# Optimization experiments

Hardware: AMD Instinct MI355X
Metric: run time of the kernel (lower is better)

The kernel has to match this reference:

```python
import jax, jax.numpy as jnp
import numpy as np

DIM = 768
NUM_HEADS = 12
HEAD_DIM = DIM // NUM_HEADS
H = W = 64
RANK = 4
LORA_SCALING = 1.0 / RANK  # lora_alpha(=1) / r


def setup_inputs() -> dict:
    key = jax.random.key(0)
    ks = jax.random.split(key, 11)
    s = 0.02
    return {
        "x": jax.random.normal(ks[0], (1, H, W, DIM), dtype=jnp.float32),
        "W_qkv": jax.random.normal(ks[1], (3 * DIM, DIM), dtype=jnp.float32) * s,
        "b_qkv": jax.random.normal(ks[2], (3 * DIM,), dtype=jnp.float32) * s,
        "A_q": jax.random.normal(ks[3], (RANK, DIM), dtype=jnp.float32) * s,
        "B_q": jax.random.normal(ks[4], (DIM, RANK), dtype=jnp.float32) * s,
        "A_v": jax.random.normal(ks[5], (RANK, DIM), dtype=jnp.float32) * s,
        "B_v": jax.random.normal(ks[6], (DIM, RANK), dtype=jnp.float32) * s,
        "rel_h": jax.random.normal(ks[7], (2 * H - 1, HEAD_DIM), dtype=jnp.float32) * s,
        "rel_w": jax.random.normal(ks[8], (2 * W - 1, HEAD_DIM), dtype=jnp.float32) * s,
        "W_proj": jax.random.normal(ks[9], (DIM, DIM), dtype=jnp.float32) * s,
        "b_proj": jax.random.normal(ks[10], (DIM,), dtype=jnp.float32) * s,
    }


def _get_rel_pos(size, rel_pos):
    # q_size == k_size == size; relative coords indexed into (2*size-1, head_dim)
    coords = jnp.arange(size)[:, None] - jnp.arange(size)[None, :] + (size - 1)
    return rel_pos[coords]  # (size, size, head_dim)


def reference(x, W_qkv, b_qkv, A_q, B_q, A_v, B_v, rel_h, rel_w, W_proj, b_proj):
    B, h, w, dim = x.shape
    nh, hd = NUM_HEADS, HEAD_DIM
    scale = hd ** -0.5
    n = h * w
    xf = x.reshape(B, n, dim)

    # LoRA-merged QKV: base linear + low-rank deltas on q and v thirds only
    qkv = xf @ W_qkv.T + b_qkv  # (B, n, 3*dim)
    dq = ((xf @ A_q.T) @ B_q.T) * LORA_SCALING
    dv = ((xf @ A_v.T) @ B_v.T) * LORA_SCALING
    qkv = qkv.at[..., :dim].add(dq).at[..., 2 * dim:].add(dv)

    qkv = qkv.reshape(B, n, 3, nh, hd).transpose(2, 0, 3, 1, 4).reshape(3, B * nh, n, hd)
    q, k, v = qkv[0], qkv[1], qkv[2]  # each (B*nh, n, hd)

    attn = (q * scale) @ jnp.swapaxes(k, -2, -1)  # (B*nh, n, n)

    # decomposed relative position bias (SAM style)
    Rh = _get_rel_pos(h, rel_h)  # (h, h, hd)
    Rw = _get_rel_pos(w, rel_w)  # (w, w, hd)
    r_q = q.reshape(B * nh, h, w, hd)
    bias_h = jnp.einsum("bhwc,hkc->bhwk", r_q, Rh)  # (B*nh, h, w, h)
    bias_w = jnp.einsum("bhwc,wkc->bhwk", r_q, Rw)  # (B*nh, h, w, w)
    attn = (attn.reshape(B * nh, h, w, h, w)
            + bias_h[:, :, :, :, None]
            + bias_w[:, :, :, None, :]).reshape(B * nh, n, n)

    attn = jax.nn.softmax(attn, axis=-1)
    out = (attn @ v).reshape(B, nh, h, w, hd).transpose(0, 2, 3, 1, 4).reshape(B, h, w, dim)
    return out @ W_proj.T + b_proj
```

## Files before the change

### kernel.cpp

```cpp
#include <hip/hip_runtime.h>

#define NTOK 4096
#define DIMD 768
#define NHD  12
#define HDD  64
#define DK   800

typedef float  f32x2  __attribute__((ext_vector_type(2)));
typedef float  f32x4  __attribute__((ext_vector_type(4)));
typedef float  f32x16 __attribute__((ext_vector_type(16)));
typedef short  s16x8  __attribute__((ext_vector_type(8)));

#define MFMA16(a, b, c) __builtin_amdgcn_mfma_f32_16x16x32_bf16(a, b, c, 0, 0, 0)
#define MFMA32(a, b, c) __builtin_amdgcn_mfma_f32_32x32x16_bf16(a, b, c, 0, 0, 0)

#if __has_builtin(__builtin_amdgcn_exp2f)
#define EXP2(x) __builtin_amdgcn_exp2f(x)
#else
#define EXP2(x) exp2f(x)
#endif

__device__ inline short f2b(float f) {
  unsigned u = __float_as_uint(f);
  u += 0x7FFFu + ((u >> 16) & 1u);
  return (short)(u >> 16);
}
__device__ inline float b2f(short s) {
  return __uint_as_float(((unsigned)(unsigned short)s) << 16);
}
__device__ inline void gl_lds16(const short* g, short* l) {
  __builtin_amdgcn_global_load_lds(
      (const __attribute__((address_space(1))) unsigned int*)g,
      (__attribute__((address_space(3))) unsigned int*)l, 16, 0, 0);
}


__global__ __launch_bounds__(64)
void k_prep_w(const float* __restrict__ Wqkv, const float* __restrict__ Bq,
              const float* __restrict__ Bv, const float* __restrict__ Wp,
              short* __restrict__ we, short* __restrict__ wpb) {
  const int j = blockIdx.x;
  const int l = threadIdx.x;
  if (j < 2304) {
#pragma unroll
    for (int k = 0; k < 12; ++k)
      we[(size_t)j * DK + l + 64 * k] = f2b(Wqkv[(size_t)j * DIMD + l + 64 * k]);
    if (l < 32) {
      int c = 768 + l;
      short v = 0;
      if (l < 4) {
        if (j < 768) v = f2b(Bq[j * 4 + l]);
      } else if (l < 8) {
        if (j >= 1536) v = f2b(Bv[(j - 1536) * 4 + (l - 4)]);
      }
      we[(size_t)j * DK + c] = v;
    }
  } else {
    const int jr = j - 2304;
#pragma unroll
    for (int k = 0; k < 12; ++k)
      wpb[(size_t)jr * DIMD + l + 64 * k] =
          f2b(Wp[(size_t)jr * DIMD + l + 64 * k]);
  }
}

__global__ __launch_bounds__(64)
void k_prep_x(const float* __restrict__ x, const float* __restrict__ Aq,
              const float* __restrict__ Av, short* __restrict__ xe) {
  const int i = blockIdx.x;
  const int l = threadIdx.x;
  float xv[12];
#pragma unroll
  for (int k = 0; k < 12; ++k) xv[k] = x[(size_t)i * DIMD + l + 64 * k];
#pragma unroll
  for (int k = 0; k < 12; ++k)
    xe[(size_t)i * DK + l + 64 * k] = f2b(xv[k]);
  float a8[8];
#pragma unroll
  for (int o = 0; o < 8; ++o) {
    const float* A = (o < 4) ? (Aq + o * DIMD) : (Av + (o - 4) * DIMD);
    float acc = 0.f;
#pragma unroll
    for (int k = 0; k < 12; ++k) acc = fmaf(xv[k], A[l + 64 * k], acc);
#pragma unroll
    for (int off = 32; off; off >>= 1) acc += __shfl_xor(acc, off, 64);
    a8[o] = acc;
  }
  if (l < 32) {
    float v = 0.f;
#pragma unroll
    for (int o = 0; o < 8; ++o)
      if (l == o) v = 0.25f * a8[o];
    xe[(size_t)i * DK + 768 + l] = (l < 8) ? f2b(v) : (short)0;
  }
}

__global__ __launch_bounds__(256)
void k_qkv(const short* __restrict__ xe, const short* __restrict__ we,
           const float* __restrict__ bqkv, short* __restrict__ qkvb,
           short* __restrict__ vtb) {
  const int j0 = blockIdx.x * 128;
  const int i0 = blockIdx.y * 128;
  __shared__ short As[128 * 32];
  __shared__ short Bs[128 * 32];
  __shared__ short Cs[128 * 130];
  const int t = threadIdx.x, lane = t & 63, w = t >> 6;
  const int l15 = lane & 15, quad = lane >> 4;
  const int wm = w >> 1, wn = w & 1;

  f32x4 acc[4][4];
#pragma unroll
  for (int a = 0; a < 4; ++a)
#pragma unroll
    for (int b = 0; b < 4; ++b) acc[a][b] = (f32x4){0.f, 0.f, 0.f, 0.f};

  for (int kk = 0; kk < DK; kk += 32) {
    __syncthreads();
#pragma unroll
    for (int rep = 0; rep < 2; ++rep) {
      int c = rep * 256 + w * 64 + lane;
      gl_lds16(xe + (size_t)(i0 + (c >> 2)) * DK + kk + (c & 3) * 8,
               &As[(rep * 256 + w * 64) * 8]);
      gl_lds16(we + (size_t)(j0 + (c >> 2)) * DK + kk + (c & 3) * 8,
               &Bs[(rep * 256 + w * 64) * 8]);
    }
    __syncthreads();
    s16x8 af[4], bf[4];
#pragma unroll
    for (int mt = 0; mt < 4; ++mt)
      af[mt] = *(const s16x8*)&As[(wm * 64 + mt * 16 + l15) * 32 + quad * 8];
#pragma unroll
    for (int nt = 0; nt < 4; ++nt)
      bf[nt] = *(const s16x8*)&Bs[(wn * 64 + nt * 16 + l15) * 32 + quad * 8];
#pragma unroll
    for (int mt = 0; mt < 4; ++mt)
#pragma unroll
      for (int nt = 0; nt < 4; ++nt)
        acc[mt][nt] = MFMA16(af[mt], bf[nt], acc[mt][nt]);
  }

  const int which = j0 / DIMD;
  float bj[4];
#pragma unroll
  for (int nt = 0; nt < 4; ++nt) bj[nt] = bqkv[j0 + wn * 64 + nt * 16 + l15];

#pragma unroll
  for (int mt = 0; mt < 4; ++mt)
#pragma unroll
    for (int r = 0; r < 4; ++r) {
      const int row = wm * 64 + mt * 16 + quad * 4 + r;
#pragma unroll
      for (int nt = 0; nt < 4; ++nt) {
        const int col = wn * 64 + nt * 16 + l15;
        Cs[row * 130 + col] = f2b(acc[mt][nt][r] + bj[nt]);
      }
    }
  __syncthreads();
  const int base_head = (j0 - which * DIMD) >> 6;
  if (which != 2) {
#pragma unroll
    for (int rp = 0; rp < 8; ++rp) {
      int f = t + 256 * rp;
      int row = f >> 4, ch = f & 15;
      int head = base_head + (ch >> 3);
      int ddb = (ch & 7) * 8;
      s16x8 v = *(const s16x8*)&Cs[row * 130 + ch * 8];
      *(s16x8*)&qkvb[(((size_t)which * NHD + head) * NTOK + i0 + row) * HDD + ddb] = v;
    }
  } else {
#pragma unroll
    for (int rp = 0; rp < 8; ++rp) {
      int f = t + 256 * rp;
      int dcol = f >> 4, n8 = (f & 15) * 8;
      unsigned wds[4];
#pragma unroll
      for (int m = 0; m < 4; ++m) {
        int s0 = n8 + 2 * m, s1 = s0 + 1;
        int sr0 = (s0 & 0x70) | ((((s0 >> 2) & 3) == 1 ? 2 : ((s0 >> 2) & 3) == 2 ? 1 : ((s0 >> 2) & 3)) << 2) | (s0 & 3);
        int sr1 = (s1 & 0x70) | ((((s1 >> 2) & 3) == 1 ? 2 : ((s1 >> 2) & 3) == 2 ? 1 : ((s1 >> 2) & 3)) << 2) | (s1 & 3);
        unsigned lo = (unsigned short)Cs[sr0 * 130 + dcol];
        unsigned hi = (unsigned short)Cs[sr1 * 130 + dcol];
        wds[m] = lo | (hi << 16);
      }
      short* dst = vtb + ((size_t)(base_head * 64) + dcol) * NTOK + i0 + n8;
      *(int4*)dst = *(int4*)&wds[0];
    }
  }
}

__global__ __launch_bounds__(256)
void k_attn7(const short* __restrict__ qkvb, const short* __restrict__ vtb,
             const float* __restrict__ relh, const float* __restrict__ relw,
             short* __restrict__ attnb) {
  const int head = blockIdx.y;
  const int hq = blockIdx.x;
  const int n0 = hq * 64;

  __shared__ short sm[20480];
  short* smb = sm;

  const short* qg  = qkvb + (size_t)(0 * NHD + head) * NTOK * HDD;
  const short* kg  = qkvb + (size_t)(1 * NHD + head) * NTOK * HDD;
  const short* vtg = vtb + (size_t)head * HDD * NTOK;

  const int t = threadIdx.x;
  const int w = t >> 6, lane = t & 63;
  const int l31 = lane & 31, h = lane >> 5;
  const int kh = w >> 1, qh = w & 1;
  const int q = qh * 32 + l31;

  const int slot = w * 64 + lane;
  const int krow = slot >> 3;
  const int kcol = ((slot & 7) ^ (krow & 7)) * 8;
  const short* gK0 = kg + (size_t)krow * HDD + kcol;
  const short* gK1 = gK0 + 32 * HDD;
  const short* gV0 = vtg + (size_t)krow * NTOK + kcol;
  const short* gV1 = gV0 + (size_t)32 * NTOK;

  s16x8 qb[4];
#pragma unroll
  for (int s = 0; s < 4; ++s)
    qb[s] = *(const s16x8*)&qg[(size_t)(n0 + q) * HDD + s * 16 + 8 * h];

#pragma unroll
  for (int rp = 0; rp < 4; ++rp) {
    int f = t + 256 * rp;
    int d = f >> 3, c = (f & 7) * 8;
    float4 v0 = make_float4(0, 0, 0, 0), v1 = v0;
    if (d < 127) {
      const float* s_ = relw + (size_t)d * HDD + c;
      v0 = *(const float4*)s_; v1 = *(const float4*)(s_ + 4);
    }
    short4 b0, b1;
    b0.x = f2b(v0.x); b0.y = f2b(v0.y); b0.z = f2b(v0.z); b0.w = f2b(v0.w);
    b1.x = f2b(v1.x); b1.y = f2b(v1.y); b1.z = f2b(v1.z); b1.w = f2b(v1.w);
    *(short4*)&smb[d * 72 + c] = b0;
    *(short4*)&smb[d * 72 + c + 4] = b1;
  }
  __syncthreads();

  f32x16 mc0 = (f32x16)(0.f), mc1 = (f32x16)(0.f);
#pragma unroll
  for (int s = 0; s < 4; ++s) {
    s16x8 a0 = *(const s16x8*)&smb[((kh * 2) * 32 + l31) * 72 + s * 16 + 8 * h];
    s16x8 a1 = *(const s16x8*)&smb[((kh * 2 + 1) * 32 + l31) * 72 + s * 16 + 8 * h];
    mc0 = MFMA32(a0, qb[s], mc0);
    mc1 = MFMA32(a1, qb[s], mc1);
  }
  __syncthreads();
#pragma unroll
  for (int reg = 0; reg < 16; ++reg) {
    int dl = (reg & 3) + 8 * (reg >> 2) + 4 * h;
    smb[(kh * 64 + dl) * 64 + q] = f2b(mc0[reg] * 1.44269504f);
    smb[(kh * 64 + 32 + dl) * 64 + q] = f2b(mc1[reg] * 1.44269504f);
  }
  __syncthreads();

  f32x2 bw2[8];
#pragma unroll
  for (int i = 0; i < 8; ++i)
#pragma unroll
    for (int p = 0; p < 2; ++p) {
      int reg = 2 * i + p;
      int kl64 = kh * 32 + (reg & 3) + 8 * (reg >> 2) + 4 * h;
      int dneed = q - kl64 + 63;
      bw2[i][p] = b2f(smb[dneed * 64 + q]);
    }
  __syncthreads();

#pragma unroll
  for (int rp = 0; rp < 2; ++rp) {
    int f = t + 256 * rp;
    int kt = f >> 3, c = (f & 7) * 8;
    const float* s_ = relh + (size_t)(hq + 63 - kt) * HDD + c;
    float4 v0 = *(const float4*)s_, v1 = *(const float4*)(s_ + 4);
    short4 b0, b1;
    b0.x = f2b(v0.x); b0.y = f2b(v0.y); b0.z = f2b(v0.z); b0.w = f2b(v0.w);
    b1.x = f2b(v1.x); b1.y = f2b(v1.y); b1.z = f2b(v1.z); b1.w = f2b(v1.w);
    *(short4*)&smb[kt * 72 + c] = b0;
    *(short4*)&smb[kt * 72 + c + 4] = b1;
  }
  __syncthreads();

  f32x16 hc = (f32x16)(0.f);
#pragma unroll
  for (int s = 0; s < 4; ++s) {
    s16x8 a = *(const s16x8*)&smb[(kh * 32 + l31) * 72 + s * 16 + 8 * h];
    hc = MFMA32(a, qb[s], hc);
  }
#pragma unroll
  for (int reg = 0; reg < 16; ++reg) {
    int ktl = kh * 32 + (reg & 3) + 8 * (reg >> 2) + 4 * h;
    smb[16384 + ktl * 64 + q] = f2b(hc[reg] * 1.44269504f);
  }
  __syncthreads();

  gl_lds16(gK0, smb + 0 + w * 512);
  gl_lds16(gK1, smb + 2048 + w * 512);
  gl_lds16(gV0, smb + 8192 + w * 512);
  gl_lds16(gV1, smb + 8192 + 2048 + w * 512);
  gK0 += 4096; gK1 += 4096;
  gV0 += 64; gV1 += 64;

  int baseS[4], baseV[2];
#pragma unroll
  for (int s = 0; s < 4; ++s)
    baseS[s] = (kh * 32 + l31) * 64 + (((2 * s + h) ^ (l31 & 7)) * 8);
#pragma unroll
  for (int s2 = 0; s2 < 2; ++s2)
    baseV[s2] = l31 * 64 + (((kh * 4 + s2 * 2 + h) ^ (l31 & 7)) * 8);

  f32x2 ps2 = (f32x2)(0.f);
  f32x16 oc0 = (f32x16)(0.f), oc1 = (f32x16)(0.f);

#define ATTN_ITER(KT, KSRC, VSRC, KDST, VDST)                                  \
  {                                                                            \
    __syncthreads();                                                           \
    if ((KT) < 63) {                                                           \
      gl_lds16(gK0, smb + (KDST) + w * 512);                                   \
      gl_lds16(gK1, smb + (KDST) + 2048 + w * 512);                            \
      gl_lds16(gV0, smb + (VDST) + w * 512);                                   \
      gl_lds16(gV1, smb + (VDST) + 2048 + w * 512);                            \
      gK0 += 4096; gK1 += 4096; gV0 += 64; gV1 += 64;                          \
    }                                                                          \
    f32x16 sc_ = (f32x16)(0.f);                                                \
    _Pragma("unroll") for (int s = 0; s < 4; ++s) {                            \
      s16x8 a = *(const s16x8*)&smb[(KSRC) + baseS[s]];                        \
      sc_ = MFMA32(a, qb[s], sc_);                                             \
    }                                                                          \
    float bhl2 = b2f(smb[16384 + (KT) * 64 + q]);                              \
    unsigned pk[8];                                                            \
    _Pragma("unroll") for (int i = 0; i < 8; ++i) {                            \
      f32x2 s2;                                                                \
      s2[0] = sc_[2 * i]; s2[1] = sc_[2 * i + 1];                              \
      f32x2 r = s2 * 0.18033688f + (bw2[i] + bhl2);                            \
      float e0 = EXP2(r[0]);                                                   \
      float e1 = EXP2(r[1]);                                                   \
      f32x2 e2; e2[0] = e0; e2[1] = e1;                                        \
      ps2 += e2;                                                               \
      pk[i] = __builtin_amdgcn_perm(__float_as_uint(e1),                       \
                                    __float_as_uint(e0), 0x07060302u);         \
    }                                                                          \
    _Pragma("unroll") for (int s2i = 0; s2i < 2; ++s2i) {                      \
      union { unsigned u[4]; s16x8 v; } B;                                     \
      B.u[0] = pk[4 * s2i + 0];                                                \
      B.u[1] = pk[4 * s2i + 1];                                                \
      B.u[2] = pk[4 * s2i + 2];                                                \
      B.u[3] = pk[4 * s2i + 3];                                                \
      s16x8 a0 = *(const s16x8*)&smb[(VSRC) + baseV[s2i]];                     \
      s16x8 a1 = *(const s16x8*)&smb[(VSRC) + 2048 + baseV[s2i]];              \
      oc0 = MFMA32(a0, B.v, oc0);                                              \
      oc1 = MFMA32(a1, B.v, oc1);                                              \
    }                                                                          \
  }

  for (int k2 = 0; k2 < 32; ++k2) {
    ATTN_ITER(2 * k2,     0,    8192,  4096, 12288);
    ATTN_ITER(2 * k2 + 1, 4096, 12288, 0,    8192);
  }
#undef ATTN_ITER

  __syncthreads();
  float ps = ps2[0] + ps2[1];
  float* obuf = (float*)smb;
  float* psb  = (float*)smb + 4224;
  short* tbuf = smb + 8576;
  ps += __shfl_xor(ps, 32, 64);
  if (kh == 1) {
#pragma unroll
    for (int reg = 0; reg < 16; ++reg) {
      int dl = (reg & 3) + 8 * (reg >> 2) + 4 * h;
      obuf[dl * 66 + q] = oc0[reg];
      obuf[(32 + dl) * 66 + q] = oc1[reg];
    }
    if (lane < 32) psb[q] = ps;
  }
  __syncthreads();
  if (kh == 0) {
    float inv = 1.f / (ps + psb[q]);
#pragma unroll
    for (int reg = 0; reg < 16; ++reg) {
      int dl = (reg & 3) + 8 * (reg >> 2) + 4 * h;
      tbuf[dl * 66 + q] = f2b((oc0[reg] + obuf[dl * 66 + q]) * inv);
      tbuf[(32 + dl) * 66 + q] = f2b((oc1[reg] + obuf[(32 + dl) * 66 + q]) * inv);
    }
  }
  __syncthreads();
  {
    int qq = t >> 2, seg = t & 3;
    unsigned wds[8];
#pragma unroll
    for (int m = 0; m < 8; ++m) {
      unsigned lo = (unsigned short)tbuf[(seg * 16 + 2 * m) * 66 + qq];
      unsigned hi = (unsigned short)tbuf[(seg * 16 + 2 * m + 1) * 66 + qq];
      wds[m] = lo | (hi << 16);
    }
    short* dst = attnb + (size_t)(n0 + qq) * DIMD + head * 64 + seg * 16;
    *(int4*)dst = *(int4*)&wds[0];
    *(int4*)(dst + 8) = *(int4*)&wds[4];
  }
}

__global__ __launch_bounds__(256)
void k_proj(const short* __restrict__ ab, const short* __restrict__ wpb,
            const float* __restrict__ bp, float* __restrict__ out) {
  const int j0 = blockIdx.x * 64;
  const int i0 = blockIdx.y * 128;
  __shared__ short As[128 * 32];
  __shared__ short Bs[64 * 32];
  const int t = threadIdx.x, lane = t & 63, w = t >> 6;
  const int l15 = lane & 15, quad = lane >> 4;
  const int wm = w >> 1, wn = w & 1;

  f32x4 acc[4][2];
#pragma unroll
  for (int a = 0; a < 4; ++a)
#pragma unroll
    for (int b = 0; b < 2; ++b) acc[a][b] = (f32x4){0.f, 0.f, 0.f, 0.f};

  for (int kk = 0; kk < DIMD; kk += 32) {
    __syncthreads();
#pragma unroll
    for (int rep = 0; rep < 2; ++rep) {
      int c = rep * 256 + w * 64 + lane;
      gl_lds16(ab + (size_t)(i0 + (c >> 2)) * DIMD + kk + (c & 3) * 8,
               &As[(rep * 256 + w * 64) * 8]);
    }
    {
      gl_lds16(wpb + (size_t)(j0 + ((w * 64 + lane) >> 2)) * DIMD + kk +
                   ((w * 64 + lane) & 3) * 8,
               &Bs[(w * 64) * 8]);
    }
    __syncthreads();
    s16x8 af[4], bf[2];
#pragma unroll
    for (int mt = 0; mt < 4; ++mt)
      af[mt] = *(const s16x8*)&As[(wm * 64 + mt * 16 + l15) * 32 + quad * 8];
#pragma unroll
    for (int nt = 0; nt < 2; ++nt)
      bf[nt] = *(const s16x8*)&Bs[(wn * 32 + nt * 16 + l15) * 32 + quad * 8];
#pragma unroll
    for (int mt = 0; mt < 4; ++mt)
#pragma unroll
      for (int nt = 0; nt < 2; ++nt)
        acc[mt][nt] = MFMA16(af[mt], bf[nt], acc[mt][nt]);
  }

#pragma unroll
  for (int mt = 0; mt < 4; ++mt)
#pragma unroll
    for (int r = 0; r < 4; ++r) {
      const int i = i0 + wm * 64 + mt * 16 + quad * 4 + r;
#pragma unroll
      for (int nt = 0; nt < 2; ++nt) {
        const int j = j0 + wn * 32 + nt * 16 + l15;
        out[(size_t)i * DIMD + j] = acc[mt][nt][r] + bp[j];
      }
    }
}

extern "C" void kernel_launch(void* const* d_in, const int* in_sizes, int n_in,
                              void* d_out, int out_size, void* d_ws, size_t ws_size,
                              hipStream_t stream) {
  (void)in_sizes; (void)n_in; (void)out_size; (void)ws_size;
  const float* x    = (const float*)d_in[0];
  const float* Wqkv = (const float*)d_in[1];
  const float* bqkv = (const float*)d_in[2];
  const float* Aq   = (const float*)d_in[3];
  const float* Bq   = (const float*)d_in[4];
  const float* Av   = (const float*)d_in[5];
  const float* Bv   = (const float*)d_in[6];
  const float* relh = (const float*)d_in[7];
  const float* relw = (const float*)d_in[8];
  const float* Wp   = (const float*)d_in[9];
  const float* bp   = (const float*)d_in[10];
  float* out = (float*)d_out;

  float* ws = (float*)d_ws;
  short* xe    = (short*)(ws);
  short* we    = (short*)(ws + 1638400);
  short* wpb   = (short*)(ws + 2560000);
  short* qkvb  = (short*)(ws + 2854912);
  short* vtb   = (short*)(ws + 7573504);
  short* attnb = (short*)(ws + 9146368);

  k_prep_w<<<dim3(3072), dim3(64), 0, stream>>>(Wqkv, Bq, Bv, Wp, we, wpb);
  k_prep_x<<<dim3(NTOK), dim3(64), 0, stream>>>(x, Aq, Av, xe);
  k_qkv<<<dim3(18, 32), dim3(256), 0, stream>>>(xe, we, bqkv, qkvb, vtb);
  k_attn7<<<dim3(64, NHD), dim3(256), 0, stream>>>(qkvb, vtb, relh, relw, attnb);
  k_proj<<<dim3(12, 32), dim3(256), 0, stream>>>(attnb, wpb, bp, out);
}
```

Before: 220.4 us.

## Split attention over key range with atomic-counter merge; fuse prep kernels

Attention now runs as a split-K style kernel. Each query tile and head is split into two blocks over halves of the key range, which doubles the grid from 768 to 1536 blocks and fills the CUs better. Each block writes an unnormalized bf16 partial output and its row sums to workspace. The last block to arrive, detected with an atomic counter, combines the two partials and normalizes them. The two prep kernels are merged into one launch that also zeroes the counters. The cost is extra global traffic for the partials, bf16 rounding of the partial sums, and the lack of a max-subtraction softmax shared across splits, which depends on the existing fixed-offset scheme.

```diff
diff --git a/kernel.cpp b/kernel.cpp
--- a/kernel.cpp
+++ b/kernel.cpp
@@ -36,9 +36,12 @@
 
 
 __global__ __launch_bounds__(64)
-void k_prep_w(const float* __restrict__ Wqkv, const float* __restrict__ Bq,
-              const float* __restrict__ Bv, const float* __restrict__ Wp,
-              short* __restrict__ we, short* __restrict__ wpb) {
+void k_prep(const float* __restrict__ Wqkv, const float* __restrict__ Bq,
+            const float* __restrict__ Bv, const float* __restrict__ Wp,
+            const float* __restrict__ x, const float* __restrict__ Aq,
+            const float* __restrict__ Av, short* __restrict__ we,
+            short* __restrict__ wpb, short* __restrict__ xe,
+            unsigned* __restrict__ cnt) {
   const int j = blockIdx.x;
   const int l = threadIdx.x;
   if (j < 2304) {
@@ -55,43 +58,41 @@
       }
       we[(size_t)j * DK + c] = v;
     }
-  } else {
+  } else if (j < 3072) {
     const int jr = j - 2304;
 #pragma unroll
     for (int k = 0; k < 12; ++k)
       wpb[(size_t)jr * DIMD + l + 64 * k] =
           f2b(Wp[(size_t)jr * DIMD + l + 64 * k]);
-  }
-}
-
-__global__ __launch_bounds__(64)
-void k_prep_x(const float* __restrict__ x, const float* __restrict__ Aq,
-              const float* __restrict__ Av, short* __restrict__ xe) {
-  const int i = blockIdx.x;
-  const int l = threadIdx.x;
-  float xv[12];
-#pragma unroll
-  for (int k = 0; k < 12; ++k) xv[k] = x[(size_t)i * DIMD + l + 64 * k];
-#pragma unroll
-  for (int k = 0; k < 12; ++k)
-    xe[(size_t)i * DK + l + 64 * k] = f2b(xv[k]);
-  float a8[8];
-#pragma unroll
-  for (int o = 0; o < 8; ++o) {
-    const float* A = (o < 4) ? (Aq + o * DIMD) : (Av + (o - 4) * DIMD);
-    float acc = 0.f;
-#pragma unroll
-    for (int k = 0; k < 12; ++k) acc = fmaf(xv[k], A[l + 64 * k], acc);
-#pragma unroll
-    for (int off = 32; off; off >>= 1) acc += __shfl_xor(acc, off, 64);
-    a8[o] = acc;
-  }
-  if (l < 32) {
-    float v = 0.f;
-#pragma unroll
-    for (int o = 0; o < 8; ++o)
-      if (l == o) v = 0.25f * a8[o];
-    xe[(size_t)i * DK + 768 + l] = (l < 8) ? f2b(v) : (short)0;
+  } else if (j < 7168) {
+    const int i = j - 3072;
+    float xv[12];
+#pragma unroll
+    for (int k = 0; k < 12; ++k) xv[k] = x[(size_t)i * DIMD + l + 64 * k];
+#pragma unroll
+    for (int k = 0; k < 12; ++k)
+      xe[(size_t)i * DK + l + 64 * k] = f2b(xv[k]);
+    float a8[8];
+#pragma unroll
+    for (int o = 0; o < 8; ++o) {
+      const float* A = (o < 4) ? (Aq + o * DIMD) : (Av + (o - 4) * DIMD);
+      float acc = 0.f;
+#pragma unroll
+      for (int k = 0; k < 12; ++k) acc = fmaf(xv[k], A[l + 64 * k], acc);
+#pragma unroll
+      for (int off = 32; off; off >>= 1) acc += __shfl_xor(acc, off, 64);
+      a8[o] = acc;
+    }
+    if (l < 32) {
+      float v = 0.f;
+#pragma unroll
+      for (int o = 0; o < 8; ++o)
+        if (l == o) v = 0.25f * a8[o];
+      xe[(size_t)i * DK + 768 + l] = (l < 8) ? f2b(v) : (short)0;
+    }
+  } else {
+#pragma unroll
+    for (int k = 0; k < 12; ++k) cnt[l + 64 * k] = 0u;
   }
 }
 
@@ -189,12 +190,15 @@
 }
 
 __global__ __launch_bounds__(256)
-void k_attn7(const short* __restrict__ qkvb, const short* __restrict__ vtb,
+void k_attn8(const short* __restrict__ qkvb, const short* __restrict__ vtb,
              const float* __restrict__ relh, const float* __restrict__ relw,
-             short* __restrict__ attnb) {
+             short* __restrict__ po, float* __restrict__ pps,
+             unsigned* __restrict__ cnt, short* __restrict__ attnb) {
   const int head = blockIdx.y;
   const int hq = blockIdx.x;
+  const int z = blockIdx.z;
   const int n0 = hq * 64;
+  const int pair = head * 64 + hq;
 
   __shared__ short sm[20480];
   short* smb = sm;
@@ -208,13 +212,14 @@
   const int l31 = lane & 31, h = lane >> 5;
   const int kh = w >> 1, qh = w & 1;
   const int q = qh * 32 + l31;
+  const int kt0 = z * 32;
 
   const int slot = w * 64 + lane;
   const int krow = slot >> 3;
   const int kcol = ((slot & 7) ^ (krow & 7)) * 8;
-  const short* gK0 = kg + (size_t)krow * HDD + kcol;
+  const short* gK0 = kg + ((size_t)kt0 * 64 + krow) * HDD + kcol;
   const short* gK1 = gK0 + 32 * HDD;
-  const short* gV0 = vtg + (size_t)krow * NTOK + kcol;
+  const short* gV0 = vtg + (size_t)krow * NTOK + kt0 * 64 + kcol;
   const short* gV1 = gV0 + (size_t)32 * NTOK;
 
   s16x8 qb[4];
@@ -268,11 +273,9 @@
     }
   __syncthreads();
 
-#pragma unroll
-  for (int rp = 0; rp < 2; ++rp) {
-    int f = t + 256 * rp;
-    int kt = f >> 3, c = (f & 7) * 8;
-    const float* s_ = relh + (size_t)(hq + 63 - kt) * HDD + c;
+  {
+    int kt = t >> 3, c = (t & 7) * 8;
+    const float* s_ = relh + (size_t)(hq + 63 - (kt0 + kt)) * HDD + c;
     float4 v0 = *(const float4*)s_, v1 = *(const float4*)(s_ + 4);
     short4 b0, b1;
     b0.x = f2b(v0.x); b0.y = f2b(v0.y); b0.z = f2b(v0.z); b0.w = f2b(v0.w);
@@ -282,16 +285,20 @@
   }
   __syncthreads();
 
-  f32x16 hc = (f32x16)(0.f);
-#pragma unroll
-  for (int s = 0; s < 4; ++s) {
-    s16x8 a = *(const s16x8*)&smb[(kh * 32 + l31) * 72 + s * 16 + 8 * h];
-    hc = MFMA32(a, qb[s], hc);
-  }
-#pragma unroll
-  for (int reg = 0; reg < 16; ++reg) {
-    int ktl = kh * 32 + (reg & 3) + 8 * (reg >> 2) + 4 * h;
-    smb[16384 + ktl * 64 + q] = f2b(hc[reg] * 1.44269504f);
+  {
+    f32x16 hc = (f32x16)(0.f);
+#pragma unroll
+    for (int s = 0; s < 4; ++s) {
+      s16x8 a = *(const s16x8*)&smb[l31 * 72 + s * 16 + 8 * h];
+      hc = MFMA32(a, qb[s], hc);
+    }
+    if (kh == 0) {
+#pragma unroll
+      for (int reg = 0; reg < 16; ++reg) {
+        int ktl = (reg & 3) + 8 * (reg >> 2) + 4 * h;
+        smb[16384 + ktl * 64 + q] = f2b(hc[reg] * 1.44269504f);
+      }
+    }
   }
   __syncthreads();
 
@@ -316,7 +323,7 @@
 #define ATTN_ITER(KT, KSRC, VSRC, KDST, VDST)                                  \
   {                                                                            \
     __syncthreads();                                                           \
-    if ((KT) < 63) {                                                           \
+    if ((KT) < 31) {                                                           \
       gl_lds16(gK0, smb + (KDST) + w * 512);                                   \
       gl_lds16(gK1, smb + (KDST) + 2048 + w * 512);                            \
       gl_lds16(gV0, smb + (VDST) + w * 512);                                   \
@@ -354,7 +361,7 @@
     }                                                                          \
   }
 
-  for (int k2 = 0; k2 < 32; ++k2) {
+  for (int k2 = 0; k2 < 16; ++k2) {
     ATTN_ITER(2 * k2,     0,    8192,  4096, 12288);
     ATTN_ITER(2 * k2 + 1, 4096, 12288, 0,    8192);
   }
@@ -365,6 +372,8 @@
   float* obuf = (float*)smb;
   float* psb  = (float*)smb + 4224;
   short* tbuf = smb + 8576;
+  int*   flg  = (int*)(smb + 12800);
+  float* fin  = (float*)(smb + 13056);
   ps += __shfl_xor(ps, 32, 64);
   if (kh == 1) {
 #pragma unroll
@@ -376,14 +385,43 @@
     if (lane < 32) psb[q] = ps;
   }
   __syncthreads();
+  short* pob = po + ((size_t)pair * 2 + z) * 4096;
   if (kh == 0) {
-    float inv = 1.f / (ps + psb[q]);
 #pragma unroll
     for (int reg = 0; reg < 16; ++reg) {
       int dl = (reg & 3) + 8 * (reg >> 2) + 4 * h;
-      tbuf[dl * 66 + q] = f2b((oc0[reg] + obuf[dl * 66 + q]) * inv);
-      tbuf[(32 + dl) * 66 + q] = f2b((oc1[reg] + obuf[(32 + dl) * 66 + q]) * inv);
-    }
+      pob[dl * 64 + q] = f2b(oc0[reg] + obuf[dl * 66 + q]);
+      pob[(32 + dl) * 64 + q] = f2b(oc1[reg] + obuf[(32 + dl) * 66 + q]);
+    }
+    if (h == 0) pps[((size_t)pair * 2 + z) * 64 + q] = ps + psb[q];
+  }
+  __threadfence();
+  __syncthreads();
+  if (t == 0) {
+    unsigned old = atomicAdd(&cnt[pair], 1u);
+    *flg = (int)old;
+  }
+  __syncthreads();
+  if (*flg != 1) return;
+  __threadfence();
+
+  if (t < 64) {
+    float s0 = pps[((size_t)pair * 2 + 0) * 64 + t];
+    float s1 = pps[((size_t)pair * 2 + 1) * 64 + t];
+    fin[t] = 1.f / (s0 + s1);
+  }
+  __syncthreads();
+  const short* po0 = po + ((size_t)pair * 2 + 0) * 4096;
+  const short* po1 = po + ((size_t)pair * 2 + 1) * 4096;
+#pragma unroll
+  for (int rp = 0; rp < 2; ++rp) {
+    int f = t + 256 * rp;
+    int d = f >> 3, q8 = (f & 7) * 8;
+    s16x8 a = *(const s16x8*)&po0[d * 64 + q8];
+    s16x8 b = *(const s16x8*)&po1[d * 64 + q8];
+#pragma unroll
+    for (int jj = 0; jj < 8; ++jj)
+      tbuf[d * 66 + q8 + jj] = f2b((b2f(a[jj]) + b2f(b[jj])) * fin[q8 + jj]);
   }
   __syncthreads();
   {
@@ -483,10 +521,14 @@
   short* qkvb  = (short*)(ws + 2854912);
   short* vtb   = (short*)(ws + 7573504);
   short* attnb = (short*)(ws + 9146368);
-
-  k_prep_w<<<dim3(3072), dim3(64), 0, stream>>>(Wqkv, Bq, Bv, Wp, we, wpb);
-  k_prep_x<<<dim3(NTOK), dim3(64), 0, stream>>>(x, Aq, Av, xe);
+  short* po    = (short*)(ws + 10719232);
+  float* pps   = (float*)(ws + 13864960);
+  unsigned* cnt = (unsigned*)(ws + 13963264);
+
+  k_prep<<<dim3(7169), dim3(64), 0, stream>>>(Wqkv, Bq, Bv, Wp, x, Aq, Av,
+                                              we, wpb, xe, cnt);
   k_qkv<<<dim3(18, 32), dim3(256), 0, stream>>>(xe, we, bqkv, qkvb, vtb);
-  k_attn7<<<dim3(64, NHD), dim3(256), 0, stream>>>(qkvb, vtb, relh, relw, attnb);
+  k_attn8<<<dim3(64, NHD, 2), dim3(256), 0, stream>>>(qkvb, vtb, relh, relw,
+                                                      po, pps, cnt, attnb);
   k_proj<<<dim3(12, 32), dim3(256), 0, stream>>>(attnb, wpb, bp, out);
 }
```

After: 430.3 us. 1.95x slower.
